# Optimization experiments

Hardware: AMD Instinct MI355X
Metric: run time of the kernel (lower is better)

Reference implementation:

```python
import jax, jax.numpy as jnp
import numpy as np
from jax import lax

B_SZ, C_IN, C_OUT, H_IM, W_IM = 2, 128, 128, 64, 64
N_STATE = 16
DT_RANK = 4  # ceil(128/32)


def _ln_cf(x, w, b, eps=1e-6):
    # channels_first LayerNorm over channel dim
    u = x.mean(1, keepdims=True)
    s = ((x - u) ** 2).mean(1, keepdims=True)
    return w[None, :, None, None] * (x - u) / jnp.sqrt(s + eps) + b[None, :, None, None]


def _bn_train(x, g, b, eps=1e-5):
    # BatchNorm2d in training mode (batch statistics, biased variance)
    m = x.mean((0, 2, 3), keepdims=True)
    v = ((x - m) ** 2).mean((0, 2, 3), keepdims=True)
    return g[None, :, None, None] * (x - m) / jnp.sqrt(v + eps) + b[None, :, None, None]


def _dwconv(x, w, b):
    y = lax.conv_general_dilated(x, w, (1, 1), 'SAME', feature_group_count=x.shape[1],
                                 dimension_numbers=('NCHW', 'OIHW', 'NCHW'))
    return y + b[None, :, None, None]


def _conv1x1(x, w, b):
    return jnp.einsum('oi,bihw->bohw', w, x) + b[None, :, None, None]


def _selective_scan(u, dt, A, Bm, Cm, D, delta_bias):
    # u, dt: [B,Ch,L]; A: [Ch,N]; Bm, Cm: [B,N,L]; D: [Ch]
    dt = jax.nn.softplus(dt + delta_bias[None, :, None])
    xs = (dt.transpose(2, 0, 1), u.transpose(2, 0, 1), Bm.transpose(2, 0, 1), Cm.transpose(2, 0, 1))
    h0 = jnp.zeros(u.shape[:2] + (A.shape[1],), u.dtype)

    def step(h, inp):
        dt_t, u_t, b_t, c_t = inp
        dA = jnp.exp(dt_t[..., None] * A)                        # [B,Ch,N]
        h = h * dA + (dt_t * u_t)[..., None] * b_t[:, None, :]   # [B,Ch,N]
        return h, jnp.einsum('bcn,bn->bc', h, c_t)

    _, ys = lax.scan(step, h0, xs)
    return ys.transpose(1, 2, 0) + u * D[None, :, None]


def _ssm_apply(u, Wx, bx, Wdt, bdt, Alog, D, r):
    # u: [B,Ch,L]. Replicates torch row-major .reshape of [(B L),D] -> [B,D,L].
    Bb, Ch, L = u.shape
    N = Alog.shape[1]
    x_flat = u.transpose(0, 2, 1).reshape(Bb * L, Ch)   # 'b c l -> (b l) c'
    x_dbl = x_flat @ Wx.T + bx
    dt = (x_dbl[:, :r] @ Wdt.T + bdt).reshape(Bb, Wdt.shape[0], L)
    Bm = x_dbl[:, r:r + N].reshape(Bb, N, L)
    Cm = x_dbl[:, r + N:].reshape(Bb, N, L)
    return _selective_scan(u, dt, -jnp.exp(Alog), Bm, Cm, D, bdt)


def _forward(x, ln_in_w, ln_in_b, inproj_w, inproj_b, ln_mamba_w, ln_mamba_b, convm_w, convm_b,
             convr_w, convr_b, ln_cat_w, ln_cat_b, xproj_f_w, xproj_f_b, dtproj_f_w, dtproj_f_b,
             Alog_f, D_f, xproj_b_w, xproj_b_b, dtproj_b_w, dtproj_b_b, Alog_b, D_b,
             xproj_u_w, xproj_u_b, dtproj_u_w, dtproj_u_b, Alog_u, D_u, gate1_w, gate1_b,
             bn_g, bn_b, gate2_w, gate2_b, outproj_w, outproj_b, outln_w, outln_b):
    Bb, C, H, W = x.shape
    L = H * W
    half = C // 2
    x = _ln_cf(x, ln_in_w, ln_in_b)
    xp = _conv1x1(x, inproj_w, inproj_b)
    x_mamba, x_res = xp[:, :C], xp[:, C:]
    x_mamba = _ln_cf(x_mamba, ln_mamba_w, ln_mamba_b)
    x_mamba = jax.nn.silu(_dwconv(x_mamba, convm_w, convm_b))
    x_res = jax.nn.silu(_dwconv(x_res, convr_w, convr_b))
    # forward scan on first half of channels
    xf = x_mamba[:, :half].reshape(Bb, half, L)
    yf = _ssm_apply(xf, xproj_f_w, xproj_f_b, dtproj_f_w, dtproj_f_b, Alog_f, D_f, DT_RANK).reshape(Bb, half, H, W)
    # backward scan on second half (flip H,W, scan, flip back)
    xb = x_mamba[:, half:][:, :, ::-1, ::-1]
    yb = _ssm_apply(xb.reshape(Bb, half, L), xproj_b_w, xproj_b_b, dtproj_b_w, dtproj_b_b,
                    Alog_b, D_b, DT_RANK).reshape(Bb, half, H, W)[:, :, ::-1, ::-1]
    concat = _ln_cf(jnp.concatenate([yf, yb], axis=1), ln_cat_w, ln_cat_b)
    # uncertainty-ordered scan on full x_mamba
    sig = jax.nn.sigmoid(x_mamba.mean(1, keepdims=True))
    unc = (-(sig * jnp.log(sig + 1e-6))).reshape(Bb, L)
    idx = jnp.argsort(-unc, axis=1)       # descending uncertainty
    inv = jnp.argsort(idx, axis=1)        # inverse permutation
    xs = jnp.take_along_axis(x_mamba.reshape(Bb, C, L), idx[:, None, :], axis=2)
    yu = _ssm_apply(xs, xproj_u_w, xproj_u_b, dtproj_u_w, dtproj_u_b, Alog_u, D_u, 2 * DT_RANK)
    yu = jnp.take_along_axis(yu, inv[:, None, :], axis=2).reshape(Bb, C, H, W)
    # gated fusion
    g = jax.nn.relu(_bn_train(_conv1x1(jnp.concatenate([concat, yu], 1), gate1_w, gate1_b), bn_g, bn_b))
    g = jax.nn.sigmoid(_conv1x1(g, gate2_w, gate2_b))
    fused = g * yu + (1.0 - g) * concat
    out = _conv1x1(jnp.concatenate([fused, x_res], 1), outproj_w, outproj_b)
    return _ln_cf(out, outln_w, outln_b)


def setup_inputs() -> dict:
    key = jax.random.key(0)
    ks = jax.random.split(key, 16)
    C, half, R, N = C_IN, C_IN // 2, DT_RANK, N_STATE
    rn = lambda k, shp, s=0.02: jax.random.normal(k, shp, jnp.float32) * s

    def inv_dt(k, n):
        dt = jnp.exp(jax.random.uniform(k, (n,)) * (np.log(0.1) - np.log(0.001)) + np.log(0.001))
        dt = jnp.maximum(dt, 1e-4)
        return dt + jnp.log(-jnp.expm1(-dt))

    std = R ** -0.5
    Alog_h = jnp.log(jnp.broadcast_to(jnp.arange(1, N + 1, dtype=jnp.float32), (half, N)))
    Alog_fl = jnp.log(jnp.broadcast_to(jnp.arange(1, N + 1, dtype=jnp.float32), (C, N)))
    return {
        'x': jax.random.normal(ks[0], (B_SZ, C, H_IM, W_IM), jnp.float32),
        'ln_in_w': jnp.ones(C), 'ln_in_b': jnp.zeros(C),
        'inproj_w': rn(ks[1], (2 * C, C)), 'inproj_b': jnp.zeros(2 * C),
        'ln_mamba_w': jnp.ones(C), 'ln_mamba_b': jnp.zeros(C),
        'convm_w': rn(ks[2], (C, 1, 3, 3), 0.1), 'convm_b': jnp.zeros(C),
        'convr_w': rn(ks[3], (C, 1, 3, 3), 0.1), 'convr_b': jnp.zeros(C),
        'ln_cat_w': jnp.ones(C), 'ln_cat_b': jnp.zeros(C),
        'xproj_f_w': rn(ks[4], (R + 2 * N, half)), 'xproj_f_b': jnp.zeros(R + 2 * N),
        'dtproj_f_w': jax.random.uniform(ks[5], (half, R), minval=-std, maxval=std),
        'dtproj_f_b': inv_dt(ks[6], half),
        'Alog_f': Alog_h, 'D_f': jnp.ones(half),
        'xproj_b_w': rn(ks[7], (R + 2 * N, half)), 'xproj_b_b': jnp.zeros(R + 2 * N),
        'dtproj_b_w': jax.random.uniform(ks[8], (half, R), minval=-std, maxval=std),
        'dtproj_b_b': inv_dt(ks[9], half),
        'Alog_b': Alog_h, 'D_b': jnp.ones(half),
        'xproj_u_w': rn(ks[10], (2 * R + 2 * N, C)), 'xproj_u_b': jnp.zeros(2 * R + 2 * N),
        'dtproj_u_w': jax.random.uniform(ks[11], (C, 2 * R), minval=-std, maxval=std),
        'dtproj_u_b': inv_dt(ks[12], C),
        'Alog_u': Alog_fl, 'D_u': jnp.ones(C),
        'gate1_w': rn(ks[13], (C, 2 * C)), 'gate1_b': jnp.zeros(C),
        'bn_g': jnp.ones(C), 'bn_b': jnp.zeros(C),
        'gate2_w': rn(ks[14], (C, C)), 'gate2_b': jnp.zeros(C),
        'outproj_w': rn(ks[15], (C_OUT, 2 * C)), 'outproj_b': jnp.zeros(C_OUT),
        'outln_w': jnp.ones(C_OUT), 'outln_b': jnp.zeros(C_OUT),
    }


def reference(x, ln_in_w, ln_in_b, inproj_w, inproj_b, ln_mamba_w, ln_mamba_b, convm_w, convm_b,
              convr_w, convr_b, ln_cat_w, ln_cat_b, xproj_f_w, xproj_f_b, dtproj_f_w, dtproj_f_b,
              Alog_f, D_f, xproj_b_w, xproj_b_b, dtproj_b_w, dtproj_b_b, Alog_b, D_b,
              xproj_u_w, xproj_u_b, dtproj_u_w, dtproj_u_b, Alog_u, D_u, gate1_w, gate1_b,
              bn_g, bn_b, gate2_w, gate2_b, outproj_w, outproj_b, outln_w, outln_b):
    return _forward(x, ln_in_w, ln_in_b, inproj_w, inproj_b, ln_mamba_w, ln_mamba_b, convm_w, convm_b,
                    convr_w, convr_b, ln_cat_w, ln_cat_b, xproj_f_w, xproj_f_b, dtproj_f_w, dtproj_f_b,
                    Alog_f, D_f, xproj_b_w, xproj_b_b, dtproj_b_w, dtproj_b_b, Alog_b, D_b,
                    xproj_u_w, xproj_u_b, dtproj_u_w, dtproj_u_b, Alog_u, D_u, gate1_w, gate1_b,
                    bn_g, bn_b, gate2_w, gate2_b, outproj_w, outproj_b, outln_w, outln_b)
```

## Files before the change

### kernel.cpp

```cpp
#include <hip/hip_runtime.h>
#include <cstdint>
#include <cstddef>

#define TPB 256

namespace {

constexpr int B_SZ = 2;
constexpr int C    = 128;
constexpr int HALF = 64;
constexpr int L    = 4096;
constexpr int N    = 16;
constexpr int HH   = 64;
constexpr int WW   = 64;
constexpr int ROW  = 48;

__device__ __forceinline__ float softplusf(float x) {
  return fmaxf(x, 0.f) + __logf(1.f + __expf(-fabsf(x)));
}
__device__ __forceinline__ float sigm(float x) { return 1.f / (1.f + __expf(-x)); }

__device__ __forceinline__ unsigned long long unc_key(float u, int i) {
  unsigned m = __float_as_uint(u);
  m = (m & 0x80000000u) ? ~m : (m | 0x80000000u);
  return ((unsigned long long)(~m) << 32) | (unsigned)i;
}

__global__ void k_pixln(const float* __restrict__ X, const float* __restrict__ w,
                        const float* __restrict__ bchan, float* __restrict__ Y) {
  const int px = threadIdx.x & 31;
  const int g  = threadIdx.x >> 5;
  const int p  = blockIdx.x * 32 + px;
  const int b  = p / L, l = p % L;
  const float* Xp = X + (size_t)b * C * L + l;
  float v[16];
  float s = 0.f, s2 = 0.f;
#pragma unroll
  for (int j = 0; j < 16; ++j) {
    float t = Xp[(size_t)(g * 16 + j) * L];
    v[j] = t; s += t; s2 += t * t;
  }
  __shared__ float red[2][8][32];
  red[0][g][px] = s; red[1][g][px] = s2;
  __syncthreads();
  float st = 0.f, qt = 0.f;
#pragma unroll
  for (int k = 0; k < 8; ++k) { st += red[0][k][px]; qt += red[1][k][px]; }
  const float m = st * (1.f / C);
  const float r = rsqrtf(qt * (1.f / C) - m * m + 1e-6f);
  float* Yp = Y + (size_t)b * C * L + l;
#pragma unroll
  for (int j = 0; j < 16; ++j) {
    int c = g * 16 + j;
    Yp[(size_t)c * L] = w[c] * (v[j] - m) * r + bchan[c];
  }
}

__global__ void k_lncat(const float* __restrict__ yf, const float* __restrict__ yb,
                        const float* __restrict__ w, const float* __restrict__ bchan,
                        float* __restrict__ Y) {
  const int px = threadIdx.x & 31;
  const int g  = threadIdx.x >> 5;
  const int p  = blockIdx.x * 32 + px;
  const int b  = p / L, l = p % L;
  float v[16];
  float s = 0.f, s2 = 0.f;
#pragma unroll
  for (int j = 0; j < 16; ++j) {
    int c = g * 16 + j;
    float t = (c < 64) ? yf[((size_t)b * HALF + c) * L + l]
                       : yb[((size_t)b * HALF + (c - 64)) * L + (L - 1 - l)];
    v[j] = t; s += t; s2 += t * t;
  }
  __shared__ float red[2][8][32];
  red[0][g][px] = s; red[1][g][px] = s2;
  __syncthreads();
  float st = 0.f, qt = 0.f;
#pragma unroll
  for (int k = 0; k < 8; ++k) { st += red[0][k][px]; qt += red[1][k][px]; }
  const float m = st * (1.f / C);
  const float r = rsqrtf(qt * (1.f / C) - m * m + 1e-6f);
  float* Yp = Y + (size_t)b * C * L + l;
#pragma unroll
  for (int j = 0; j < 16; ++j) {
    int c = g * 16 + j;
    Yp[(size_t)c * L] = w[c] * (v[j] - m) * r + bchan[c];
  }
}

__global__ void k_conv_in(const float* __restrict__ X,
                          const float* __restrict__ W, const float* __restrict__ bias,
                          float* __restrict__ Y,
                          float* __restrict__ st1s, float* __restrict__ st1q) {
  constexpr int O_PB = 8;
  __shared__ float Wl[O_PB * 128];
  const int o0 = blockIdx.y * O_PB;
  const int b  = blockIdx.z;
  for (int t = threadIdx.x; t < O_PB * 128; t += TPB) {
    int i = t / O_PB, k = t % O_PB;
    Wl[t] = W[(size_t)(o0 + k) * 128 + i];
  }
  __syncthreads();
  const int l = blockIdx.x * TPB + threadIdx.x;
  const float* X0 = X + (size_t)b * C * L + l;
  float acc[O_PB];
#pragma unroll
  for (int k = 0; k < O_PB; ++k) acc[k] = bias[o0 + k];
#pragma unroll 8
  for (int i = 0; i < 128; ++i) {
    float xv = X0[(size_t)i * L];
#pragma unroll
    for (int k = 0; k < O_PB; ++k) acc[k] += Wl[i * O_PB + k] * xv;
  }
#pragma unroll
  for (int k = 0; k < O_PB; ++k)
    Y[((size_t)b * 256 + o0 + k) * L + l] = acc[k];
  if (o0 < 128) {
    float ss = 0.f, qq = 0.f;
#pragma unroll
    for (int k = 0; k < O_PB; ++k) { ss += acc[k]; qq += acc[k] * acc[k]; }
    atomicAdd(&st1s[b * L + l], ss);
    atomicAdd(&st1q[b * L + l], qq);
  }
}

__global__ void k_dwconv_t(const float* __restrict__ xp,
                           const float* __restrict__ st1s, const float* __restrict__ st1q,
                           const float* __restrict__ lnw, const float* __restrict__ lnb,
                           const float* __restrict__ Wm, const float* __restrict__ bm,
                           const float* __restrict__ Wr, const float* __restrict__ br,
                           float* __restrict__ xm, float* __restrict__ xr) {
  const int c = blockIdx.y;
  const int z = blockIdx.z;
  const int b = z & 1, mode = z >> 1;
  const int h0 = blockIdx.x * 4;
  __shared__ float T[6][66];
  const float* Xc = xp + ((size_t)b * 2 * C + (mode ? C + c : c)) * L;
  const float lw = mode ? 0.f : lnw[c];
  const float lb2 = mode ? 0.f : lnb[c];
  for (int t = threadIdx.x; t < 6 * 66; t += TPB) {
    int r = t / 66, cc = t % 66 - 1;
    int hh = h0 - 1 + r;
    float v = 0.f;
    if (hh >= 0 && hh < HH && cc >= 0 && cc < WW) {
      int li = hh * WW + cc;
      v = Xc[li];
      if (mode == 0) {
        float sv = st1s[b * L + li], qv = st1q[b * L + li];
        float m = sv * (1.f / 128.f);
        float rr = rsqrtf(qv * (1.f / 128.f) - m * m + 1e-6f);
        v = (v - m) * rr * lw + lb2;
      }
    }
    T[r][t % 66] = v;
  }
  __syncthreads();
  const int hl = threadIdx.x >> 6, w = threadIdx.x & 63;
  const float* W9 = (mode ? Wr : Wm) + c * 9;
  float acc = mode ? br[c] : bm[c];
#pragma unroll
  for (int kh = 0; kh < 3; ++kh)
#pragma unroll
    for (int kw = 0; kw < 3; ++kw)
      acc += T[hl + kh][w + kw] * W9[kh * 3 + kw];
  const int l = (h0 + hl) * WW + w;
  float* Yp = mode ? xr : xm;
  Yp[((size_t)b * C + c) * L + l] = acc * sigm(acc);
}

__global__ void k_unc(const float* __restrict__ xm, float* __restrict__ unc) {
  const int lp = threadIdx.x & 63;
  const int wv = threadIdx.x >> 6;
  const int p  = blockIdx.x * 64 + lp;
  const int b = p / L, l = p % L;
  const float* Xp = xm + (size_t)b * C * L + l;
  float s = 0.f;
#pragma unroll 8
  for (int i = 0; i < 32; ++i) s += Xp[(size_t)(wv * 32 + i) * L];
  __shared__ float r1[4][64];
  r1[wv][lp] = s;
  __syncthreads();
  if (wv == 0) {
    float st = r1[0][lp] + r1[1][lp] + r1[2][lp] + r1[3][lp];
    float sg = sigm(st / C);
    unc[p] = -(sg * __logf(sg + 1e-6f));
  }
}

__global__ void k_rank(const float* __restrict__ unc, int* __restrict__ rankbuf) {
  constexpr int JC = 512;
  __shared__ unsigned long long K[JC];
  const int b  = blockIdx.z;
  const int j0 = blockIdx.y * JC;
  const int i  = blockIdx.x * TPB + threadIdx.x;
  for (int t = threadIdx.x; t < JC; t += TPB)
    K[t] = unc_key(unc[b * L + j0 + t], j0 + t);
  __syncthreads();
  const unsigned long long my = unc_key(unc[b * L + i], i);
  int cnt = 0;
#pragma unroll 8
  for (int j = 0; j < JC; ++j) cnt += (K[j] < my) ? 1 : 0;
  atomicAdd(&rankbuf[b * L + i], cnt);
}

__global__ void k_scatgath(const float* __restrict__ xm, const int* __restrict__ rankbuf,
                           float* __restrict__ xs, int* __restrict__ idx) {
  int t = blockIdx.x * TPB + threadIdx.x;
  int l = t % L, c = (t / L) % C, b = t / (C * L);
  int r = rankbuf[b * L + l];
  xs[((size_t)b * C + c) * L + r] = xm[t];
  if (c == 0) idx[b * L + r] = l;
}

__global__ void k_convx_all(const float* __restrict__ xm, const float* __restrict__ xs,
                            const float* __restrict__ Wf, const float* __restrict__ bf,
                            const float* __restrict__ Wb, const float* __restrict__ bb,
                            const float* __restrict__ Wu, const float* __restrict__ bu,
                            float* __restrict__ XDF, float* __restrict__ XDU) {
  const int z = blockIdx.z;
  const bool isU = z >= 4;
  const int I = isU ? 128 : 64;
  const int O = isU ? 40 : 36;
  const int RT = isU ? 8 : 4;
  const int o0 = blockIdx.y * 4;
  if (o0 >= O) return;
  int b, dir;
  const float *W, *bi;
  if (!isU) { dir = z >> 1; b = z & 1; W = dir ? Wb : Wf; bi = dir ? bb : bf; }
  else      { dir = 0; b = z - 4; W = Wu; bi = bu; }
  __shared__ float Wl[4 * 128];
  for (int t = threadIdx.x; t < 4 * I; t += TPB) {
    int i = t / 4, k = t % 4;
    Wl[t] = W[(size_t)(o0 + k) * I + i];
  }
  __syncthreads();
  const int l = blockIdx.x * TPB + threadIdx.x;
  const int ls = isU ? l : (dir ? (L - 1 - l) : l);
  const float* Xb = isU ? (xs + (size_t)b * C * L)
                        : (xm + ((size_t)b * C + dir * HALF) * L);
  float acc[4];
#pragma unroll
  for (int k = 0; k < 4; ++k) acc[k] = bi[o0 + k];
#pragma unroll 8
  for (int i = 0; i < I; ++i) {
    float xv = Xb[(size_t)i * L + ls];
#pragma unroll
    for (int k = 0; k < 4; ++k) acc[k] += Wl[i * 4 + k] * xv;
  }
  const int slot0 = (o0 < RT) ? o0 : o0 + (16 - RT);
  float* yp = isU ? (XDU + ((size_t)b * L + l) * ROW + slot0)
                  : (XDF + ((size_t)z * L + l) * ROW + slot0);
#pragma unroll
  for (int k = 0; k < 4; ++k) yp[k] = acc[k];
}

__global__ __launch_bounds__(1024) void
k_scan_all(const float* __restrict__ xdblF, const float* __restrict__ xdblU,
           const float* __restrict__ dtf_w, const float* __restrict__ dtf_b,
           const float* __restrict__ dtb_w, const float* __restrict__ dtb_b,
           const float* __restrict__ dtu_w, const float* __restrict__ dtu_b,
           const float* __restrict__ xm, const float* __restrict__ xs,
           const int* __restrict__ idx,
           const float* __restrict__ Alog_f, const float* __restrict__ Alog_b,
           const float* __restrict__ Alog_u,
           const float* __restrict__ D_f, const float* __restrict__ D_b,
           const float* __restrict__ D_u,
           float* __restrict__ yf, float* __restrict__ yb, float* __restrict__ yu) {
  const int blk = blockIdx.x;
  const int tid = threadIdx.x;
  const bool isU = blk >= 256;
  int CsT, RT, c, b, dir;
  const float *Wdt, *bdt, *Alog, *Dv, *xdbl, *Ub;
  const int* idxb = nullptr;
  float* Y;
  if (!isU) {
    CsT = 64; RT = 4;
    int zb = blk >> 6; c = blk & 63; dir = zb >> 1; b = zb & 1;
    Wdt = dir ? dtb_w : dtf_w; bdt = dir ? dtb_b : dtf_b;
    Alog = dir ? Alog_b : Alog_f; Dv = dir ? D_b : D_f;
    xdbl = xdblF + (size_t)zb * L * ROW;
    Ub = xm + ((size_t)b * C + dir * HALF + c) * L;
    Y = (dir ? yb : yf) + ((size_t)b * HALF + c) * L;
  } else {
    CsT = 128; RT = 8;
    int blk2 = blk - 256; b = blk2 >> 7; c = blk2 & 127; dir = 0;
    Wdt = dtu_w; bdt = dtu_b; Alog = Alog_u; Dv = D_u;
    xdbl = xdblU + (size_t)b * L * ROW;
    Ub = xs + ((size_t)b * C + c) * L;
    idxb = idx + b * L;
    Y = yu + ((size_t)b * C + c) * L;
  }
  __shared__ float sW[1024];
  __shared__ float sb2[128];
  __shared__ float4 dtL4[64 * 17];
  __shared__ float4 uL4[64 * 17];
  __shared__ float sA[N][65], sH[N][65];
  for (int t = tid; t < CsT * RT; t += 1024) {
    int csrc = t / RT, r = t % RT;
    sW[r * CsT + csrc] = Wdt[t];
  }
  for (int t = tid; t < CsT; t += 1024) sb2[t] = bdt[t];
  __syncthreads();
  {
    const int chunk_d = tid >> 4;
    const int sq4 = tid & 15;
    const int sq = sq4 * 4;
    const int lsrc = isU ? (c * 32 + (chunk_d >> 1)) : (c * 64 + chunk_d);
    const float* xrp = xdbl + (size_t)lsrc * ROW;
    float xr[8];
    for (int r = 0; r < RT; ++r) xr[r] = xrp[r];
    const float bcc = sb2[c];
    float dv[4], uv[4];
#pragma unroll
    for (int j = 0; j < 4; ++j) {
      int s = sq + j;
      int csrc = isU ? (((chunk_d & 1) << 6) + s) : s;
      float acc = sb2[csrc] + bcc;
      for (int r = 0; r < RT; ++r) acc += sW[r * CsT + csrc] * xr[r];
      int l = (chunk_d << 6) + s;
      dv[j] = softplusf(acc);
      uv[j] = Ub[isU ? l : (dir ? (L - 1 - l) : l)];
    }
    dtL4[chunk_d * 17 + sq4] = make_float4(dv[0], dv[1], dv[2], dv[3]);
    uL4[chunk_d * 17 + sq4]  = make_float4(uv[0], uv[1], uv[2], uv[3]);
  }
  __syncthreads();
  const int n = tid & 15;
  const int chunk = tid >> 4;
  const float a = -__expf(Alog[c * N + n]);
  const float* bp = xdbl + ((size_t)(chunk << 6)) * ROW + 16 + n;
  const float* cp = bp + 16;
  float ap = 1.f, h = 0.f;
#pragma unroll 4
  for (int m = 0; m < 16; ++m) {
    float4 d4 = dtL4[chunk * 17 + m];
    float4 u4 = uL4[chunk * 17 + m];
    float dv[4] = {d4.x, d4.y, d4.z, d4.w};
    float uv[4] = {u4.x, u4.y, u4.z, u4.w};
#pragma unroll
    for (int jj = 0; jj < 4; ++jj) {
      int s = (m << 2) + jj;
      float bn = bp[(size_t)s * ROW];
      float dA = __expf(dv[jj] * a);
      ap *= dA;
      h = h * dA + dv[jj] * uv[jj] * bn;
    }
  }
  sA[n][chunk] = ap; sH[n][chunk] = h;
  __syncthreads();
  {
    const int w = tid >> 6;
    const int k = tid & 63;
    float A = sA[w][k];
    float Bv = sH[w][k];
#pragma unroll
    for (int j = 1; j < 64; j <<= 1) {
      float pa = __shfl_up(A, j);
      float pb = __shfl_up(Bv, j);
      if (k >= j) { Bv = pb * A + Bv; A = pa * A; }
    }
    float hprev = __shfl_up(Bv, 1);
    sH[w][k] = (k == 0) ? 0.f : hprev;
  }
  __syncthreads();
  h = sH[n][chunk];
  const float Dc = Dv[c];
  const float* uLrow = (const float*)&uL4[chunk * 17];
  const bool h1 = (n & 1) != 0, h2 = (n & 2) != 0, h3 = (n & 4) != 0, h4 = (n & 8) != 0;
  float ybuf[4];
#pragma unroll
  for (int q = 0; q < 4; ++q) {
    float v[16];
#pragma unroll
    for (int m = 0; m < 4; ++m) {
      float4 d4 = dtL4[chunk * 17 + (q << 2) + m];
      float4 u4 = uL4[chunk * 17 + (q << 2) + m];
      float dv[4] = {d4.x, d4.y, d4.z, d4.w};
      float uv[4] = {u4.x, u4.y, u4.z, u4.w};
#pragma unroll
      for (int jj = 0; jj < 4; ++jj) {
        int s = (q << 4) + (m << 2) + jj;
        float bn = bp[(size_t)s * ROW];
        float cn = cp[(size_t)s * ROW];
        float dA = __expf(dv[jj] * a);
        h = h * dA + dv[jj] * uv[jj] * bn;
        v[(m << 2) + jj] = h * cn;
      }
    }
    float u8[8];
#pragma unroll
    for (int k2 = 0; k2 < 8; ++k2) {
      float snd = h1 ? v[2 * k2] : v[2 * k2 + 1];
      float t = __shfl_xor(snd, 1);
      u8[k2] = (h1 ? v[2 * k2 + 1] : v[2 * k2]) + t;
    }
    float u4a[4];
#pragma unroll
    for (int k2 = 0; k2 < 4; ++k2) {
      float snd = h2 ? u8[2 * k2] : u8[2 * k2 + 1];
      float t = __shfl_xor(snd, 2);
      u4a[k2] = (h2 ? u8[2 * k2 + 1] : u8[2 * k2]) + t;
    }
    float u2a[2];
#pragma unroll
    for (int k2 = 0; k2 < 2; ++k2) {
      float snd = h3 ? u4a[2 * k2] : u4a[2 * k2 + 1];
      float t = __shfl_xor(snd, 4);
      u2a[k2] = (h3 ? u4a[2 * k2 + 1] : u4a[2 * k2]) + t;
    }
    float snd = h4 ? u2a[0] : u2a[1];
    float t = __shfl_xor(snd, 8);
    float ysum = (h4 ? u2a[1] : u2a[0]) + t;
    float myu = uLrow[(q << 4) + n];
    ybuf[q] = ysum + myu * Dc;
  }
  if (!isU) {
    float* Yp = Y + (chunk << 6);
#pragma unroll
    for (int q = 0; q < 4; ++q) Yp[16 * q + n] = ybuf[q];
  } else {
    const int s0 = chunk << 6;
#pragma unroll
    for (int q = 0; q < 4; ++q) Y[idxb[s0 + 16 * q + n]] = ybuf[q];
  }
}

template <int O_PB>
__global__ void k_gate1(const float* __restrict__ ycat, const float* __restrict__ yu,
                        const float* __restrict__ W, const float* __restrict__ bias,
                        float* __restrict__ g1, float* __restrict__ bnsum) {
  __shared__ float Wl[O_PB * 256];
  __shared__ float part[2][O_PB][4];
  const int o0 = blockIdx.y * O_PB;
  const int b  = blockIdx.z;
  for (int t = threadIdx.x; t < O_PB * 256; t += TPB) {
    int i = t / O_PB, k = t % O_PB;
    Wl[t] = W[(size_t)(o0 + k) * 256 + i];
  }
  __syncthreads();
  const int l = blockIdx.x * TPB + threadIdx.x;
  const float* c0 = ycat + (size_t)b * C * L + l;
  const float* u0 = yu + (size_t)b * C * L + l;
  float acc[O_PB];
#pragma unroll
  for (int k = 0; k < O_PB; ++k) acc[k] = bias[o0 + k];
#pragma unroll 8
  for (int i = 0; i < 128; ++i) {
    float cv = c0[(size_t)i * L];
#pragma unroll
    for (int k = 0; k < O_PB; ++k) acc[k] += Wl[i * O_PB + k] * cv;
  }
#pragma unroll 8
  for (int i = 0; i < 128; ++i) {
    float xv = u0[(size_t)i * L];
#pragma unroll
    for (int k = 0; k < O_PB; ++k) acc[k] += Wl[(128 + i) * O_PB + k] * xv;
  }
#pragma unroll
  for (int k = 0; k < O_PB; ++k)
    g1[((size_t)b * C + o0 + k) * L + l] = acc[k];
  const int wv = threadIdx.x >> 6, lnn = threadIdx.x & 63;
#pragma unroll
  for (int k = 0; k < O_PB; ++k) {
    float v = acc[k];
    v += __shfl_xor(v, 1);  v += __shfl_xor(v, 2);  v += __shfl_xor(v, 4);
    v += __shfl_xor(v, 8);  v += __shfl_xor(v, 16); v += __shfl_xor(v, 32);
    if (lnn == 0) part[0][k][wv] = v;
    float q = acc[k] * acc[k];
    q += __shfl_xor(q, 1);  q += __shfl_xor(q, 2);  q += __shfl_xor(q, 4);
    q += __shfl_xor(q, 8);  q += __shfl_xor(q, 16); q += __shfl_xor(q, 32);
    if (lnn == 0) part[1][k][wv] = q;
  }
  __syncthreads();
  if (threadIdx.x < 2 * O_PB) {
    int which = threadIdx.x >= O_PB, k = threadIdx.x % O_PB;
    float v = part[which][k][0] + part[which][k][1] + part[which][k][2] + part[which][k][3];
    atomicAdd(&bnsum[which * 128 + o0 + k], v);
  }
}

template <int O_PB>
__global__ void k_gate2_fuse(const float* __restrict__ g1,
                             const float* __restrict__ bnsum,
                             const float* __restrict__ bn_g, const float* __restrict__ bn_b,
                             const float* __restrict__ W, const float* __restrict__ bias,
                             const float* __restrict__ yu, const float* __restrict__ ycat,
                             float* __restrict__ fused) {
  __shared__ float Wl[O_PB * 128];
  __shared__ float sc[128], sh[128];
  const int o0 = blockIdx.y * O_PB;
  const int b  = blockIdx.z;
  for (int t = threadIdx.x; t < O_PB * 128; t += TPB) {
    int i = t / O_PB, k = t % O_PB;
    Wl[t] = W[(size_t)(o0 + k) * 128 + i];
  }
  for (int t = threadIdx.x; t < 128; t += TPB) {
    float sv = bnsum[t], qv = bnsum[128 + t];
    float mean = sv / (B_SZ * L);
    float var  = qv / (B_SZ * L) - mean * mean;
    float scv = bn_g[t] * rsqrtf(var + 1e-5f);
    sc[t] = scv;
    sh[t] = bn_b[t] - mean * scv;
  }
  __syncthreads();
  const int l = blockIdx.x * TPB + threadIdx.x;
  const float* Xb = g1 + (size_t)b * C * L + l;
  float acc[O_PB];
#pragma unroll
  for (int k = 0; k < O_PB; ++k) acc[k] = bias[o0 + k];
#pragma unroll 8
  for (int i = 0; i < 128; ++i) {
    float v = fmaxf(Xb[(size_t)i * L] * sc[i] + sh[i], 0.f);
#pragma unroll
    for (int k = 0; k < O_PB; ++k) acc[k] += Wl[i * O_PB + k] * v;
  }
#pragma unroll
  for (int k = 0; k < O_PB; ++k) {
    int o = o0 + k;
    float g = sigm(acc[k]);
    float yuv = yu[((size_t)b * C + o) * L + l];
    float cv = ycat[((size_t)b * C + o) * L + l];
    fused[((size_t)b * C + o) * L + l] = g * yuv + (1.f - g) * cv;
  }
}

template <int O_PB>
__global__ void k_outproj(const float* __restrict__ X1, const float* __restrict__ X2,
                          const float* __restrict__ W, const float* __restrict__ bias,
                          float* __restrict__ Y,
                          float* __restrict__ st3s, float* __restrict__ st3q) {
  __shared__ float Wl[O_PB * 256];
  const int o0 = blockIdx.y * O_PB;
  const int b  = blockIdx.z;
  for (int t = threadIdx.x; t < O_PB * 256; t += TPB) {
    int i = t / O_PB, k = t % O_PB;
    Wl[t] = W[(size_t)(o0 + k) * 256 + i];
  }
  __syncthreads();
  const int l = blockIdx.x * TPB + threadIdx.x;
  const float* Xb1 = X1 + (size_t)b * C * L + l;
  const float* Xb2 = X2 + (size_t)b * C * L + l;
  float acc[O_PB];
#pragma unroll
  for (int k = 0; k < O_PB; ++k) acc[k] = bias[o0 + k];
#pragma unroll 8
  for (int i = 0; i < 128; ++i) {
    float xv = Xb1[(size_t)i * L];
#pragma unroll
    for (int k = 0; k < O_PB; ++k) acc[k] += Wl[i * O_PB + k] * xv;
  }
#pragma unroll 8
  for (int i = 0; i < 128; ++i) {
    float xv = Xb2[(size_t)i * L];
#pragma unroll
    for (int k = 0; k < O_PB; ++k) acc[k] += Wl[(128 + i) * O_PB + k] * xv;
  }
  float ss = 0.f, qq = 0.f;
#pragma unroll
  for (int k = 0; k < O_PB; ++k) {
    Y[((size_t)b * C + o0 + k) * L + l] = acc[k];
    ss += acc[k]; qq += acc[k] * acc[k];
  }
  atomicAdd(&st3s[b * L + l], ss);
  atomicAdd(&st3q[b * L + l], qq);
}

__global__ void k_ln_out(const float* __restrict__ X,
                         const float* __restrict__ st3s, const float* __restrict__ st3q,
                         const float* __restrict__ w, const float* __restrict__ bchan,
                         float* __restrict__ Y) {
  const int t  = blockIdx.x * TPB + threadIdx.x;
  const int gi = t * 4;
  const int l  = gi % L;
  const int c  = (gi / L) % C;
  const int b  = gi / (C * L);
  const float4 v  = ((const float4*)X)[t];
  const float4 s4 = *(const float4*)(st3s + b * L + l);
  const float4 q4 = *(const float4*)(st3q + b * L + l);
  const float wc = w[c], bc = bchan[c];
  float4 o;
  {
    float m = s4.x * (1.f / C);
    float r = rsqrtf(q4.x * (1.f / C) - m * m + 1e-6f);
    o.x = wc * (v.x - m) * r + bc;
  }
  {
    float m = s4.y * (1.f / C);
    float r = rsqrtf(q4.y * (1.f / C) - m * m + 1e-6f);
    o.y = wc * (v.y - m) * r + bc;
  }
  {
    float m = s4.z * (1.f / C);
    float r = rsqrtf(q4.z * (1.f / C) - m * m + 1e-6f);
    o.z = wc * (v.z - m) * r + bc;
  }
  {
    float m = s4.w * (1.f / C);
    float r = rsqrtf(q4.w * (1.f / C) - m * m + 1e-6f);
    o.w = wc * (v.w - m) * r + bc;
  }
  ((float4*)Y)[t] = o;
}

}

extern "C" void kernel_launch(void* const* d_in, const int* in_sizes, int n_in,
                              void* d_out, int out_size, void* d_ws, size_t ws_size,
                              hipStream_t stream) {
  const float* x         = (const float*)d_in[0];
  const float* ln_in_w   = (const float*)d_in[1];
  const float* ln_in_b   = (const float*)d_in[2];
  const float* inproj_w  = (const float*)d_in[3];
  const float* inproj_b  = (const float*)d_in[4];
  const float* ln_m_w    = (const float*)d_in[5];
  const float* ln_m_b    = (const float*)d_in[6];
  const float* convm_w   = (const float*)d_in[7];
  const float* convm_b   = (const float*)d_in[8];
  const float* convr_w   = (const float*)d_in[9];
  const float* convr_b   = (const float*)d_in[10];
  const float* ln_cat_w  = (const float*)d_in[11];
  const float* ln_cat_b  = (const float*)d_in[12];
  const float* xpf_w     = (const float*)d_in[13];
  const float* xpf_b     = (const float*)d_in[14];
  const float* dtf_w     = (const float*)d_in[15];
  const float* dtf_b     = (const float*)d_in[16];
  const float* Alog_f    = (const float*)d_in[17];
  const float* D_f       = (const float*)d_in[18];
  const float* xpb_w     = (const float*)d_in[19];
  const float* xpb_b     = (const float*)d_in[20];
  const float* dtb_w     = (const float*)d_in[21];
  const float* dtb_b     = (const float*)d_in[22];
  const float* Alog_b    = (const float*)d_in[23];
  const float* D_b       = (const float*)d_in[24];
  const float* xpu_w     = (const float*)d_in[25];
  const float* xpu_b     = (const float*)d_in[26];
  const float* dtu_w     = (const float*)d_in[27];
  const float* dtu_b     = (const float*)d_in[28];
  const float* Alog_u    = (const float*)d_in[29];
  const float* D_u       = (const float*)d_in[30];
  const float* gate1_w   = (const float*)d_in[31];
  const float* gate1_b   = (const float*)d_in[32];
  const float* bn_g      = (const float*)d_in[33];
  const float* bn_b      = (const float*)d_in[34];
  const float* gate2_w   = (const float*)d_in[35];
  const float* gate2_b   = (const float*)d_in[36];
  const float* outproj_w = (const float*)d_in[37];
  const float* outproj_b = (const float*)d_in[38];
  const float* outln_w   = (const float*)d_in[39];
  const float* outln_b   = (const float*)d_in[40];

  float* ws = (float*)d_ws;
  size_t off = 0;
  auto alloc = [&](size_t n) { float* p = ws + off; off += n; return p; };

  const size_t BL = (size_t)B_SZ * L;
  float* st1s  = alloc(BL);
  float* st1q  = alloc(BL);
  float* st3s  = alloc(BL);
  float* st3q  = alloc(BL);
  int*   rank  = (int*)alloc(BL);
  float* bnsum = alloc(256);
  const size_t zeroBytes = (5 * BL + 256) * sizeof(float);

  float* xln   = alloc((size_t)B_SZ * C * L);
  float* xp    = alloc((size_t)B_SZ * 2 * C * L);
  float* xm    = alloc((size_t)B_SZ * C * L);
  float* xr    = alloc((size_t)B_SZ * C * L);
  float* unc   = alloc(BL);
  int*   idx   = (int*)alloc(BL);
  float* xs    = alloc((size_t)B_SZ * C * L);
  float* xdblF = alloc((size_t)4 * L * ROW);
  float* xdblU = alloc((size_t)2 * L * ROW);
  float* yf    = alloc((size_t)B_SZ * HALF * L);
  float* yb    = alloc((size_t)B_SZ * HALF * L);
  float* yu    = alloc((size_t)B_SZ * C * L);
  float* ycat  = alloc((size_t)B_SZ * C * L);
  float* g1    = alloc((size_t)B_SZ * C * L);
  float* fused = alloc((size_t)B_SZ * C * L);
  float* outp  = alloc((size_t)B_SZ * C * L);
  (void)ws_size; (void)in_sizes; (void)n_in; (void)out_size;

  const int pixB   = B_SZ * L / 64;
  const int pixB32 = B_SZ * L / 32;
  const int elemB  = B_SZ * C * L / TPB;

  hipMemsetAsync(st1s, 0, zeroBytes, stream);
  k_pixln<<<pixB32, TPB, 0, stream>>>(x, ln_in_w, ln_in_b, xln);
  k_conv_in<<<dim3(L / TPB, 32, B_SZ), TPB, 0, stream>>>(
      xln, inproj_w, inproj_b, xp, st1s, st1q);
  k_dwconv_t<<<dim3(HH / 4, C, 2 * B_SZ), TPB, 0, stream>>>(
      xp, st1s, st1q, ln_m_w, ln_m_b, convm_w, convm_b, convr_w, convr_b, xm, xr);
  k_unc<<<pixB, TPB, 0, stream>>>(xm, unc);
  k_rank<<<dim3(L / TPB, 8, B_SZ), TPB, 0, stream>>>(unc, rank);
  k_scatgath<<<elemB, TPB, 0, stream>>>(xm, rank, xs, idx);
  k_convx_all<<<dim3(L / TPB, 10, 6), TPB, 0, stream>>>(
      xm, xs, xpf_w, xpf_b, xpb_w, xpb_b, xpu_w, xpu_b, xdblF, xdblU);
  k_scan_all<<<512, 1024, 0, stream>>>(
      xdblF, xdblU, dtf_w, dtf_b, dtb_w, dtb_b, dtu_w, dtu_b,
      xm, xs, idx, Alog_f, Alog_b, Alog_u, D_f, D_b, D_u, yf, yb, yu);
  k_lncat<<<pixB32, TPB, 0, stream>>>(yf, yb, ln_cat_w, ln_cat_b, ycat);
  k_gate1<8><<<dim3(L / TPB, 16, B_SZ), TPB, 0, stream>>>(
      ycat, yu, gate1_w, gate1_b, g1, bnsum);
  k_gate2_fuse<8><<<dim3(L / TPB, 16, B_SZ), TPB, 0, stream>>>(
      g1, bnsum, bn_g, bn_b, gate2_w, gate2_b, yu, ycat, fused);
  k_outproj<8><<<dim3(L / TPB, 16, B_SZ), TPB, 0, stream>>>(
      fused, xr, outproj_w, outproj_b, outp, st3s, st3q);
  k_ln_out<<<(B_SZ * C * L / 4) / TPB, TPB, 0, stream>>>(
      outp, st3s, st3q, outln_w, outln_b, (float*)d_out);
}
```

Before: 291.7 us.

## Read weights via uniform global loads and replace scatter with inverse-index gather

Drops the LDS weight staging and __syncthreads from all pointwise-conv kernels, so weights are read directly from global memory at block-uniform addresses that the compiler can turn into scalar loads. Replaces the per-element scatter into sorted order with a small inverse-index kernel plus a gather kernel. The gather writes coalesced output and reads scattered input, where the old scatter did the reverse. The trade is an extra launch and reliance on the scalar cache for weight reuse.

Measured after the change: 305.8 us. 4.8% more time.

```diff
diff --git a/kernel.cpp b/kernel.cpp
--- a/kernel.cpp
+++ b/kernel.cpp
@@ -93,16 +93,11 @@
                           float* __restrict__ Y,
                           float* __restrict__ st1s, float* __restrict__ st1q) {
   constexpr int O_PB = 8;
-  __shared__ float Wl[O_PB * 128];
   const int o0 = blockIdx.y * O_PB;
   const int b  = blockIdx.z;
-  for (int t = threadIdx.x; t < O_PB * 128; t += TPB) {
-    int i = t / O_PB, k = t % O_PB;
-    Wl[t] = W[(size_t)(o0 + k) * 128 + i];
-  }
-  __syncthreads();
   const int l = blockIdx.x * TPB + threadIdx.x;
   const float* X0 = X + (size_t)b * C * L + l;
+  const float* Wp = W + (size_t)o0 * 128;
   float acc[O_PB];
 #pragma unroll
   for (int k = 0; k < O_PB; ++k) acc[k] = bias[o0 + k];
@@ -110,7 +105,7 @@
   for (int i = 0; i < 128; ++i) {
     float xv = X0[(size_t)i * L];
 #pragma unroll
-    for (int k = 0; k < O_PB; ++k) acc[k] += Wl[i * O_PB + k] * xv;
+    for (int k = 0; k < O_PB; ++k) acc[k] += Wp[k * 128 + i] * xv;
   }
 #pragma unroll
   for (int k = 0; k < O_PB; ++k)
@@ -203,13 +198,25 @@
   atomicAdd(&rankbuf[b * L + i], cnt);
 }
 
-__global__ void k_scatgath(const float* __restrict__ xm, const int* __restrict__ rankbuf,
-                           float* __restrict__ xs, int* __restrict__ idx) {
-  int t = blockIdx.x * TPB + threadIdx.x;
-  int l = t % L, c = (t / L) % C, b = t / (C * L);
-  int r = rankbuf[b * L + l];
-  xs[((size_t)b * C + c) * L + r] = xm[t];
-  if (c == 0) idx[b * L + r] = l;
+__global__ void k_invidx(const int* __restrict__ rankbuf, int* __restrict__ idx) {
+  const int t = blockIdx.x * TPB + threadIdx.x;
+  const int b = t / L, l = t % L;
+  idx[b * L + rankbuf[b * L + l]] = l;
+}
+
+__global__ void k_gather(const float* __restrict__ xm, const int* __restrict__ idx,
+                         float* __restrict__ xs) {
+  const int b  = blockIdx.z;
+  const int c0 = blockIdx.y * 8;
+  const int r  = blockIdx.x * TPB + threadIdx.x;
+  const int li = idx[b * L + r];
+  const float* Xb = xm + (size_t)b * C * L;
+  float* Yb = xs + (size_t)b * C * L;
+#pragma unroll
+  for (int j = 0; j < 8; ++j) {
+    int c = c0 + j;
+    Yb[(size_t)c * L + r] = Xb[(size_t)c * L + li];
+  }
 }
 
 __global__ void k_convx_all(const float* __restrict__ xm, const float* __restrict__ xs,
@@ -228,12 +235,7 @@
   const float *W, *bi;
   if (!isU) { dir = z >> 1; b = z & 1; W = dir ? Wb : Wf; bi = dir ? bb : bf; }
   else      { dir = 0; b = z - 4; W = Wu; bi = bu; }
-  __shared__ float Wl[4 * 128];
-  for (int t = threadIdx.x; t < 4 * I; t += TPB) {
-    int i = t / 4, k = t % 4;
-    Wl[t] = W[(size_t)(o0 + k) * I + i];
-  }
-  __syncthreads();
+  const float* Wp = W + (size_t)o0 * I;
   const int l = blockIdx.x * TPB + threadIdx.x;
   const int ls = isU ? l : (dir ? (L - 1 - l) : l);
   const float* Xb = isU ? (xs + (size_t)b * C * L)
@@ -245,7 +247,7 @@
   for (int i = 0; i < I; ++i) {
     float xv = Xb[(size_t)i * L + ls];
 #pragma unroll
-    for (int k = 0; k < 4; ++k) acc[k] += Wl[i * 4 + k] * xv;
+    for (int k = 0; k < 4; ++k) acc[k] += Wp[(size_t)k * I + i] * xv;
   }
   const int slot0 = (o0 < RT) ? o0 : o0 + (16 - RT);
   float* yp = isU ? (XDU + ((size_t)b * L + l) * ROW + slot0)
@@ -429,15 +431,10 @@
 __global__ void k_gate1(const float* __restrict__ ycat, const float* __restrict__ yu,
                         const float* __restrict__ W, const float* __restrict__ bias,
                         float* __restrict__ g1, float* __restrict__ bnsum) {
-  __shared__ float Wl[O_PB * 256];
   __shared__ float part[2][O_PB][4];
   const int o0 = blockIdx.y * O_PB;
   const int b  = blockIdx.z;
-  for (int t = threadIdx.x; t < O_PB * 256; t += TPB) {
-    int i = t / O_PB, k = t % O_PB;
-    Wl[t] = W[(size_t)(o0 + k) * 256 + i];
-  }
-  __syncthreads();
+  const float* Wp = W + (size_t)o0 * 256;
   const int l = blockIdx.x * TPB + threadIdx.x;
   const float* c0 = ycat + (size_t)b * C * L + l;
   const float* u0 = yu + (size_t)b * C * L + l;
@@ -448,13 +445,13 @@
   for (int i = 0; i < 128; ++i) {
     float cv = c0[(size_t)i * L];
 #pragma unroll
-    for (int k = 0; k < O_PB; ++k) acc[k] += Wl[i * O_PB + k] * cv;
+    for (int k = 0; k < O_PB; ++k) acc[k] += Wp[(size_t)k * 256 + i] * cv;
   }
 #pragma unroll 8
   for (int i = 0; i < 128; ++i) {
     float xv = u0[(size_t)i * L];
 #pragma unroll
-    for (int k = 0; k < O_PB; ++k) acc[k] += Wl[(128 + i) * O_PB + k] * xv;
+    for (int k = 0; k < O_PB; ++k) acc[k] += Wp[(size_t)k * 256 + 128 + i] * xv;
   }
 #pragma unroll
   for (int k = 0; k < O_PB; ++k)
@@ -486,14 +483,9 @@
                              const float* __restrict__ W, const float* __restrict__ bias,
                              const float* __restrict__ yu, const float* __restrict__ ycat,
                              float* __restrict__ fused) {
-  __shared__ float Wl[O_PB * 128];
   __shared__ float sc[128], sh[128];
   const int o0 = blockIdx.y * O_PB;
   const int b  = blockIdx.z;
-  for (int t = threadIdx.x; t < O_PB * 128; t += TPB) {
-    int i = t / O_PB, k = t % O_PB;
-    Wl[t] = W[(size_t)(o0 + k) * 128 + i];
-  }
   for (int t = threadIdx.x; t < 128; t += TPB) {
     float sv = bnsum[t], qv = bnsum[128 + t];
     float mean = sv / (B_SZ * L);
@@ -503,6 +495,7 @@
     sh[t] = bn_b[t] - mean * scv;
   }
   __syncthreads();
+  const float* Wp = W + (size_t)o0 * 128;
   const int l = blockIdx.x * TPB + threadIdx.x;
   const float* Xb = g1 + (size_t)b * C * L + l;
   float acc[O_PB];
@@ -512,7 +505,7 @@
   for (int i = 0; i < 128; ++i) {
     float v = fmaxf(Xb[(size_t)i * L] * sc[i] + sh[i], 0.f);
 #pragma unroll
-    for (int k = 0; k < O_PB; ++k) acc[k] += Wl[i * O_PB + k] * v;
+    for (int k = 0; k < O_PB; ++k) acc[k] += Wp[(size_t)k * 128 + i] * v;
   }
 #pragma unroll
   for (int k = 0; k < O_PB; ++k) {
@@ -529,14 +522,9 @@
                           const float* __restrict__ W, const float* __restrict__ bias,
                           float* __restrict__ Y,
                           float* __restrict__ st3s, float* __restrict__ st3q) {
-  __shared__ float Wl[O_PB * 256];
   const int o0 = blockIdx.y * O_PB;
   const int b  = blockIdx.z;
-  for (int t = threadIdx.x; t < O_PB * 256; t += TPB) {
-    int i = t / O_PB, k = t % O_PB;
-    Wl[t] = W[(size_t)(o0 + k) * 256 + i];
-  }
-  __syncthreads();
+  const float* Wp = W + (size_t)o0 * 256;
   const int l = blockIdx.x * TPB + threadIdx.x;
   const float* Xb1 = X1 + (size_t)b * C * L + l;
   const float* Xb2 = X2 + (size_t)b * C * L + l;
@@ -547,13 +535,13 @@
   for (int i = 0; i < 128; ++i) {
     float xv = Xb1[(size_t)i * L];
 #pragma unroll
-    for (int k = 0; k < O_PB; ++k) acc[k] += Wl[i * O_PB + k] * xv;
+    for (int k = 0; k < O_PB; ++k) acc[k] += Wp[(size_t)k * 256 + i] * xv;
   }
 #pragma unroll 8
   for (int i = 0; i < 128; ++i) {
     float xv = Xb2[(size_t)i * L];
 #pragma unroll
-    for (int k = 0; k < O_PB; ++k) acc[k] += Wl[(128 + i) * O_PB + k] * xv;
+    for (int k = 0; k < O_PB; ++k) acc[k] += Wp[(size_t)k * 256 + 128 + i] * xv;
   }
   float ss = 0.f, qq = 0.f;
 #pragma unroll
@@ -682,7 +670,6 @@
 
   const int pixB   = B_SZ * L / 64;
   const int pixB32 = B_SZ * L / 32;
-  const int elemB  = B_SZ * C * L / TPB;
 
   hipMemsetAsync(st1s, 0, zeroBytes, stream);
   k_pixln<<<pixB32, TPB, 0, stream>>>(x, ln_in_w, ln_in_b, xln);
@@ -692,7 +679,8 @@
       xp, st1s, st1q, ln_m_w, ln_m_b, convm_w, convm_b, convr_w, convr_b, xm, xr);
   k_unc<<<pixB, TPB, 0, stream>>>(xm, unc);
   k_rank<<<dim3(L / TPB, 8, B_SZ), TPB, 0, stream>>>(unc, rank);
-  k_scatgath<<<elemB, TPB, 0, stream>>>(xm, rank, xs, idx);
+  k_invidx<<<B_SZ * L / TPB, TPB, 0, stream>>>(rank, idx);
+  k_gather<<<dim3(L / TPB, 16, B_SZ), TPB, 0, stream>>>(xm, idx, xs);
   k_convx_all<<<dim3(L / TPB, 10, 6), TPB, 0, stream>>>(
       xm, xs, xpf_w, xpf_b, xpb_w, xpb_b, xpu_w, xpu_b, xdblF, xdblU);
   k_scan_all<<<512, 1024, 0, stream>>>(
```
